# Kernel optimization log

Hardware: AMD Instinct MI355X
Metric: run time of the kernel (lower is better)

## Reference

```python
import jax, jax.numpy as jnp
import numpy as np

B, C, H, W = 8, 512, 32, 32


def setup_inputs() -> dict:
    key = jax.random.key(0)
    ks = jax.random.split(key, 7)
    s = 0.02  # typical conv init scale
    return {
        "x": jax.random.normal(ks[0], (B, C, H, W), dtype=jnp.float32),
        "Wq": jax.random.normal(ks[1], (C, C), dtype=jnp.float32) * s,
        "bq": jax.random.normal(ks[2], (C,), dtype=jnp.float32) * s,
        "Wk": jax.random.normal(ks[3], (C, C), dtype=jnp.float32) * s,
        "bk": jax.random.normal(ks[4], (C,), dtype=jnp.float32) * s,
        "W6": jax.random.normal(ks[5], (C, C), dtype=jnp.float32) * s,
        "b6": jax.random.normal(ks[6], (C,), dtype=jnp.float32) * s,
    }


def _gam(x, Wq, bq, Wk, bk, W6, b6):
    b, c, h, w = x.shape
    hw = h * w
    scale = 1.0 / (c ** 0.5)
    # 1x1 convs == per-pixel channel matmuls (torch conv weight [out,in,1,1])
    q = jnp.einsum('bchw,dc->bhwd', x, Wq) + bq          # [B,H,W,C]
    q = q.reshape(b * hw, c)                              # query rows
    k = jnp.einsum('bchw,dc->bdhw', x, Wk) + bk[None, :, None, None]
    k = jnp.transpose(k, (1, 0, 2, 3)).reshape(c, b * hw)  # [C, B*HW]
    xw = (q.astype(jnp.float32) @ k.astype(jnp.float32))   # [B*HW, B*HW]
    xw = xw.reshape(b * hw, b, hw)
    xw = jnp.max(xw, axis=-1)                              # max over keys' spatial dim
    xw = jnp.mean(xw, axis=-1)                             # mean over key images
    xw = xw.reshape(b, hw) * scale
    xw = jax.nn.softmax(xw, axis=-1).astype(x.dtype)
    xw = xw.reshape(b, 1, h, w)
    x5 = x * xw
    return jnp.einsum('bchw,dc->bdhw', x5, W6) + b6[None, :, None, None]


def reference(x, Wq, bq, Wk, bk, W6, b6):
    x_new = _gam(x, Wq, bq, Wk, bk, W6, b6)
    # prototype: mean over batch and spatial dims, keep channels
    x_proto = jnp.mean(x_new.astype(jnp.float32), axis=(0, 2, 3)).astype(x.dtype)
    return x * x_proto[None, :, None, None]
```

## Files before the change

### kernel.cpp

```cpp
#include <hip/hip_runtime.h>
#include <hip/hip_bf16.h>

typedef __bf16 bf16_t;
typedef __bf16 bf16x8 __attribute__((ext_vector_type(8)));
typedef float f32x4 __attribute__((ext_vector_type(4)));

#define B_   8
#define C_   512
#define HW_  1024
#define NPIX 8192

typedef __attribute__((address_space(3))) void lds_vp;
typedef const __attribute__((address_space(1))) void gbl_vp;
__device__ __forceinline__ void gload_lds16(const void* g, void* l) {
    __builtin_amdgcn_global_load_lds((gbl_vp*)g, (lds_vp*)l, 16, 0, 0);
}

__device__ __forceinline__ void stage128x64_swz(const bf16_t* __restrict__ g,
                                                bf16_t* lds, int tid) {
    int w64 = tid & ~63;
#pragma unroll
    for (int s = 0; s < 4; ++s) {
        int u = s * 256 + tid;
        int row = u >> 3;
        int kg = (u & 7) ^ (row & 7);
        const bf16_t* src = g + (size_t)row * 512 + kg * 8;
        gload_lds16((const void*)src, (void*)(lds + (size_t)(s * 256 + w64) * 8));
    }
}

__global__ void k_transpose(const float* __restrict__ x, bf16_t* __restrict__ xT,
                            const float* __restrict__ Wq, const float* __restrict__ Wk,
                            bf16_t* __restrict__ wq, bf16_t* __restrict__ wk) {
    __shared__ bf16_t tile[64 * 66];
    int p0 = blockIdx.x * 64, c0 = blockIdx.y * 64, b = blockIdx.z;
    int t = threadIdx.x;
    int widx = ((blockIdx.z * 8 + blockIdx.y) * 16 + blockIdx.x) * 256 + t;
    wq[widx] = (bf16_t)Wq[widx];
    wk[widx] = (bf16_t)Wk[widx];
#pragma unroll
    for (int s = 0; s < 16; ++s) {
        int u = s * 256 + t;
        int cr = u >> 6, pc = u & 63;
        tile[cr * 66 + pc] = (bf16_t)x[((size_t)(b * C_ + c0 + cr)) * HW_ + p0 + pc];
    }
    __syncthreads();
#pragma unroll
    for (int s = 0; s < 16; ++s) {
        int u = s * 256 + t;
        int pr = u >> 6, cc = u & 63;
        xT[((size_t)(b * HW_ + p0 + pr)) * C_ + c0 + cc] = tile[cc * 66 + pr];
    }
}

__launch_bounds__(256, 2)
__global__ void k_gemm_qk(const bf16_t* __restrict__ xT,
                          const bf16_t* __restrict__ wq, const bf16_t* __restrict__ wk,
                          const float* __restrict__ bq, const float* __restrict__ bk,
                          bf16_t* __restrict__ qo, bf16_t* __restrict__ ko) {
    __shared__ __align__(16) bf16_t As[128 * 64];
    __shared__ __align__(16) bf16_t Bs[128 * 64];
    int bid = blockIdx.x;
    int mtile = bid >> 3;
    int nt = bid & 7;
    const bf16_t* wsel = (nt < 4) ? wq : wk;
    const float*  bsel = (nt < 4) ? bq : bk;
    bf16_t*       osel = (nt < 4) ? qo : ko;
    int nb = (nt & 3) * 128;
    int i0 = mtile * 128;
    int tid = threadIdx.x;
    int lane = tid & 63, w = tid >> 6;
    int wr = w >> 1, wc = w & 1, lr = lane & 15, lg = lane >> 4;
    int kswz = (lg ^ (lr & 7)) << 4;

    f32x4 acc[4][4];
#pragma unroll
    for (int mi = 0; mi < 4; ++mi)
#pragma unroll
        for (int ni = 0; ni < 4; ++ni)
#pragma unroll
            for (int r = 0; r < 4; ++r) acc[mi][ni][r] = 0.f;

    for (int kt = 0; kt < 8; ++kt) {
        int k0 = kt * 64;
        stage128x64_swz(xT + (size_t)i0 * 512 + k0, As, tid);
        stage128x64_swz(wsel + (size_t)nb * 512 + k0, Bs, tid);
        asm volatile("s_waitcnt vmcnt(0)" ::: "memory");
        __builtin_amdgcn_s_barrier();
#pragma unroll
        for (int kk = 0; kk < 2; ++kk) {
            bf16x8 af[4], bfr[4];
#pragma unroll
            for (int mi = 0; mi < 4; ++mi)
                af[mi] = *(const bf16x8*)((const char*)As +
                    (wr * 64 + mi * 16 + lr) * 128 + (kswz ^ (kk * 64)));
#pragma unroll
            for (int ni = 0; ni < 4; ++ni)
                bfr[ni] = *(const bf16x8*)((const char*)Bs +
                    (wc * 64 + ni * 16 + lr) * 128 + (kswz ^ (kk * 64)));
#pragma unroll
            for (int mi = 0; mi < 4; ++mi)
#pragma unroll
                for (int ni = 0; ni < 4; ++ni)
                    acc[mi][ni] = __builtin_amdgcn_mfma_f32_16x16x32_bf16(
                        af[mi], bfr[ni], acc[mi][ni], 0, 0, 0);
        }
        __builtin_amdgcn_s_barrier();
    }
#pragma unroll
    for (int ni = 0; ni < 4; ++ni) {
        int col = nb + wc * 64 + ni * 16 + lr;
        float bias = bsel[col];
#pragma unroll
        for (int mi = 0; mi < 4; ++mi) {
            int rowb = i0 + wr * 64 + mi * 16 + lg * 4;
#pragma unroll
            for (int r = 0; r < 4; ++r)
                osel[(size_t)(rowb + r) * 512 + col] = (bf16_t)(acc[mi][ni][r] + bias);
        }
    }
}


#define STAGE_A(RH, D, T)                                                          \
    gload_lds16((const void*)(q + srcA + (size_t)((RH) * 128) * 512 +              \
                              ((T) & 7) * 64),                                     \
                (void*)(ldsb + (RH) * 32768 + (D) * 16384 + ldw));                 \
    gload_lds16((const void*)(q + srcA + (size_t)((RH) * 128 + 64) * 512 +         \
                              ((T) & 7) * 64),                                     \
                (void*)(ldsb + (RH) * 32768 + (D) * 16384 + 8192 + ldw));

#define STAGE_B(RH, D, T)                                                          \
    gload_lds16((const void*)(kb + srcB +                                          \
                              (size_t)(((T) >> 3) * 256 + (RH) * 128) * 512 +      \
                              ((T) & 7) * 64),                                     \
                (void*)(ldsb + 65536 + (RH) * 32768 + (D) * 16384 + ldw));         \
    gload_lds16((const void*)(kb + srcB +                                          \
                              (size_t)(((T) >> 3) * 256 + (RH) * 128 + 64) * 512 + \
                              ((T) & 7) * 64),                                     \
                (void*)(ldsb + 65536 + (RH) * 32768 + (D) * 16384 + 8192 + ldw));

#define PHASE(D, KH, MH, STAGE_STMT, VM_STMT)                                      \
    {                                                                              \
        const char* Ab = ldsb + wr * 32768 + (D) * 16384;                          \
        const char* Bb = ldsb + 65536 + (wc >> 1) * 32768 + (D) * 16384;           \
        _Pragma("unroll")                                                          \
        for (int mi = 0; mi < 4; ++mi)                                             \
            af[mi] = *(const bf16x8*)(Ab + (aswz ^ ((KH) * 64)) +                  \
                                      ((MH) * 4 + mi) * 2048);                     \
        if ((MH) == 0) {                                                           \
            _Pragma("unroll")                                                      \
            for (int ni = 0; ni < 4; ++ni)                                         \
                bf[ni] = *(const bf16x8*)(Bb + (bswz ^ ((KH) * 64)) + ni * 2048);  \
        }                                                                          \
        STAGE_STMT;                                                                \
        __builtin_amdgcn_s_setprio(1);                                             \
        _Pragma("unroll")                                                          \
        for (int mi = 0; mi < 4; ++mi)                                             \
            _Pragma("unroll")                                                      \
            for (int ni = 0; ni < 4; ++ni)                                         \
                acc[(MH) * 4 + mi][ni] = __builtin_amdgcn_mfma_f32_16x16x32_bf16(  \
                    af[mi], bf[ni], acc[(MH) * 4 + mi][ni], 0, 0, 0);              \
        __builtin_amdgcn_s_setprio(0);                                             \
        VM_STMT;                                                                   \
        __builtin_amdgcn_s_barrier();                                              \
    }

__global__ __launch_bounds__(512, 2)
void k_gemm_max8(const bf16_t* __restrict__ q, const bf16_t* __restrict__ kp,
                 float* __restrict__ Mout) {
    __shared__ __align__(16) bf16_t lds[65536];
    char* ldsb = (char*)lds;
    int bid = blockIdx.x;
    int img = bid & 7;
    int qp = bid >> 3;
    int i0 = qp * 256;
    const bf16_t* kb = kp + (size_t)img * HW_ * C_;
    int tid = threadIdx.x;
    int lane = tid & 63, w = tid >> 6;
    int wr = w >> 2, wc = w & 3;
    int lr = lane & 15, lg = lane >> 4;
    int kswz = (lg ^ (lr & 7)) << 4;
    int aswz = lr * 128 + kswz;
    int bswz = ((wc & 1) * 64 + lr) * 128 + kswz;

    int srow = tid >> 3;
    int sk = (((tid & 7) ^ ((tid >> 3) & 7))) << 3;
    size_t srcA = (size_t)(i0 + srow) * 512 + sk;
    size_t srcB = (size_t)srow * 512 + sk;
    int ldw = (tid >> 6) * 1024;

    f32x4 acc[8][4];
    bf16x8 af[4], bf[4];
    float rm[8][4];
#pragma unroll
    for (int mi = 0; mi < 8; ++mi)
#pragma unroll
        for (int ni = 0; ni < 4; ++ni)
#pragma unroll
            for (int r = 0; r < 4; ++r) acc[mi][ni][r] = 0.f;
#pragma unroll
    for (int mi = 0; mi < 8; ++mi)
#pragma unroll
        for (int r = 0; r < 4; ++r) rm[mi][r] = -3.4e38f;

    STAGE_B(0, 0, 0) STAGE_A(0, 0, 0) STAGE_B(1, 0, 0) STAGE_A(1, 0, 0)
    STAGE_B(0, 1, 1)
    asm volatile("s_waitcnt vmcnt(2)" ::: "memory");
    __builtin_amdgcn_s_barrier();

    for (int i = 0; i < 16; ++i) {
        int tb = 2 * i + 1, tc = 2 * i + 2, td = 2 * i + 3;
        bool s = (i < 15);
        PHASE(0, 0, 0, { STAGE_A(0, 1, tb) }, {})
        PHASE(0, 0, 1, { STAGE_B(1, 1, tb) }, {})
        PHASE(0, 1, 0, { STAGE_A(1, 1, tb) }, {})
        PHASE(0, 1, 1, { if (s) { STAGE_B(0, 0, tc) } },
              { if (s) { asm volatile("s_waitcnt vmcnt(2)" ::: "memory"); }
                else   { asm volatile("s_waitcnt vmcnt(0)" ::: "memory"); } })
        PHASE(1, 0, 0, { if (s) { STAGE_A(0, 0, tc) } }, {})
        PHASE(1, 0, 1, { if (s) { STAGE_B(1, 0, tc) } }, {})
        PHASE(1, 1, 0, { if (s) { STAGE_A(1, 0, tc) } }, {})
        PHASE(1, 1, 1, { if (s) { STAGE_B(0, 1, td) } },
              { if (s) { asm volatile("s_waitcnt vmcnt(2)" ::: "memory"); } })
        if ((i & 3) == 3) {
#pragma unroll
            for (int mi = 0; mi < 8; ++mi)
#pragma unroll
                for (int r = 0; r < 4; ++r) {
                    float v = fmaxf(fmaxf(acc[mi][0][r], acc[mi][1][r]),
                                    fmaxf(acc[mi][2][r], acc[mi][3][r]));
                    rm[mi][r] = fmaxf(rm[mi][r], v);
#pragma unroll
                    for (int ni = 0; ni < 4; ++ni) acc[mi][ni][r] = 0.f;
                }
        }
    }

#pragma unroll
    for (int mi = 0; mi < 8; ++mi)
#pragma unroll
        for (int r = 0; r < 4; ++r) {
            float v = rm[mi][r];
#pragma unroll
            for (int off = 1; off < 16; off <<= 1) v = fmaxf(v, __shfl_xor(v, off));
            rm[mi][r] = v;
        }
    float* sm = (float*)lds;
    if (lr == 0) {
#pragma unroll
        for (int mi = 0; mi < 8; ++mi)
#pragma unroll
            for (int r = 0; r < 4; ++r)
                sm[wc * 256 + wr * 128 + mi * 16 + lg * 4 + r] = rm[mi][r];
    }
    __syncthreads();
    if (tid < 256) {
        float v = fmaxf(fmaxf(sm[tid], sm[256 + tid]),
                        fmaxf(sm[512 + tid], sm[768 + tid]));
        Mout[(size_t)(i0 + tid) * 8 + img] = v;
    }
}

__global__ void k_softmax(const float* __restrict__ Mout, float* __restrict__ wsm) {
    int b = blockIdx.x;
    int t = threadIdx.x;
    __shared__ float red[16];
    const float scale = 0.044194173824159216f;
    float s[4];
#pragma unroll
    for (int i = 0; i < 4; ++i) {
        int p = t + i * 256;
        const float* row = &Mout[(size_t)(b * 1024 + p) * 8];
        float acc = 0.f;
#pragma unroll
        for (int j = 0; j < 8; ++j) acc += row[j];
        s[i] = acc * (scale / 8.0f);
    }
    float m = fmaxf(fmaxf(s[0], s[1]), fmaxf(s[2], s[3]));
#pragma unroll
    for (int off = 1; off < 64; off <<= 1) m = fmaxf(m, __shfl_xor(m, off));
    if ((t & 63) == 0) red[t >> 6] = m;
    __syncthreads();
    float m4 = fmaxf(fmaxf(red[0], red[1]), fmaxf(red[2], red[3]));
    float e[4], sum = 0.f;
#pragma unroll
    for (int i = 0; i < 4; ++i) { e[i] = __expf(s[i] - m4); sum += e[i]; }
#pragma unroll
    for (int off = 1; off < 64; off <<= 1) sum += __shfl_xor(sum, off);
    if ((t & 63) == 0) red[8 + (t >> 6)] = sum;
    __syncthreads();
    float tot = red[8] + red[9] + red[10] + red[11];
    float inv = 1.0f / tot;
#pragma unroll
    for (int i = 0; i < 4; ++i) wsm[b * 1024 + t + i * 256] = e[i] * inv;
}

__global__ void k_reduce_y(const float* __restrict__ x, const float* __restrict__ wsm,
                           float* __restrict__ y) {
    int c = blockIdx.x;
    int t = threadIdx.x;
    float acc = 0.f;
    for (int b = 0; b < 8; ++b) {
        const float* xb = x + ((size_t)(b * C_ + c)) * HW_;
        const float* wb = wsm + b * HW_;
#pragma unroll
        for (int i = 0; i < 4; ++i) {
            int p = t + i * 256;
            acc += xb[p] * wb[p];
        }
    }
#pragma unroll
    for (int off = 1; off < 64; off <<= 1) acc += __shfl_xor(acc, off);
    __shared__ float red[4];
    if ((t & 63) == 0) red[t >> 6] = acc;
    __syncthreads();
    if (t == 0) y[c] = (red[0] + red[1] + red[2] + red[3]) * (1.0f / 8192.0f);
}

__global__ void k_proto(const float* __restrict__ W6, const float* __restrict__ b6,
                        const float* __restrict__ y, float* __restrict__ proto) {
    int d = blockIdx.x;
    int lane = threadIdx.x;
    float acc = 0.f;
#pragma unroll
    for (int i = 0; i < 8; ++i)
        acc += W6[(size_t)d * C_ + lane + i * 64] * y[lane + i * 64];
#pragma unroll
    for (int off = 1; off < 64; off <<= 1) acc += __shfl_xor(acc, off);
    if (lane == 0) proto[d] = acc + b6[d];
}

__global__ void k_final(const float* __restrict__ x, const float* __restrict__ proto,
                        float* __restrict__ out) {
    int idx = blockIdx.x * 256 + threadIdx.x;
    float4 v = ((const float4*)x)[idx];
    int c = (idx >> 8) & 511;
    float p = proto[c];
    v.x *= p; v.y *= p; v.z *= p; v.w *= p;
    ((float4*)out)[idx] = v;
}

extern "C" void kernel_launch(void* const* d_in, const int* in_sizes, int n_in,
                              void* d_out, int out_size, void* d_ws, size_t ws_size,
                              hipStream_t stream) {
    const float* x  = (const float*)d_in[0];
    const float* Wq = (const float*)d_in[1];
    const float* bq = (const float*)d_in[2];
    const float* Wk = (const float*)d_in[3];
    const float* bk = (const float*)d_in[4];
    const float* W6 = (const float*)d_in[5];
    const float* b6 = (const float*)d_in[6];
    float* out = (float*)d_out;

    char* ws = (char*)d_ws;
    bf16_t* xT    = (bf16_t*)(ws);
    float*  Mout  = (float*)(ws);
    bf16_t* wqb   = (bf16_t*)(ws + 8388608);
    bf16_t* wkb   = (bf16_t*)(ws + 8912896);
    bf16_t* qb    = (bf16_t*)(ws + 9437184);
    bf16_t* kb    = (bf16_t*)(ws + 17825792);
    float*  wsm   = (float*)(ws + 26476544);
    float*  yv    = (float*)(ws + 26509312);
    float*  proto = (float*)(ws + 26511360);

    hipLaunchKernelGGL(k_transpose, dim3(16, 8, 8), dim3(256), 0, stream,
                       x, xT, Wq, Wk, wqb, wkb);
    hipLaunchKernelGGL(k_gemm_qk, dim3(512), dim3(256), 0, stream,
                       xT, wqb, wkb, bq, bk, qb, kb);
    hipLaunchKernelGGL(k_gemm_max8, dim3(256), dim3(512), 0, stream, qb, kb, Mout);
    hipLaunchKernelGGL(k_softmax, dim3(8), dim3(256), 0, stream, Mout, wsm);
    hipLaunchKernelGGL(k_reduce_y, dim3(512), dim3(256), 0, stream, x, wsm, yv);
    hipLaunchKernelGGL(k_proto, dim3(512), dim3(64), 0, stream, W6, b6, yv, proto);
    hipLaunchKernelGGL(k_final, dim3(4096), dim3(256), 0, stream, x, proto, out);
}
```

Baseline: 96.13 us.

## Reuse pipelined 256x256 GEMM macros for Q/K projection and vectorize transpose

Replaces the simple 128x128 single-buffered Q/K projection GEMM with a 256x256-tile, 512-thread kernel. It reuses the double-buffered STAGE/PHASE macros from the max GEMM, so global-to-LDS loads overlap with MFMA work. The transpose kernel now uses float4 loads and bf16x4 stores with a 65-stride LDS tile. The larger tiles launch only 128 blocks, which may underfill the GPU's compute units.

```diff
diff --git a/kernel.cpp b/kernel.cpp
--- a/kernel.cpp
+++ b/kernel.cpp
@@ -3,6 +3,7 @@
 
 typedef __bf16 bf16_t;
 typedef __bf16 bf16x8 __attribute__((ext_vector_type(8)));
+typedef __bf16 bf16x4 __attribute__((ext_vector_type(4)));
 typedef float f32x4 __attribute__((ext_vector_type(4)));
 
 #define B_   8
@@ -16,108 +17,36 @@
     __builtin_amdgcn_global_load_lds((gbl_vp*)g, (lds_vp*)l, 16, 0, 0);
 }
 
-__device__ __forceinline__ void stage128x64_swz(const bf16_t* __restrict__ g,
-                                                bf16_t* lds, int tid) {
-    int w64 = tid & ~63;
-#pragma unroll
-    for (int s = 0; s < 4; ++s) {
-        int u = s * 256 + tid;
-        int row = u >> 3;
-        int kg = (u & 7) ^ (row & 7);
-        const bf16_t* src = g + (size_t)row * 512 + kg * 8;
-        gload_lds16((const void*)src, (void*)(lds + (size_t)(s * 256 + w64) * 8));
-    }
-}
-
 __global__ void k_transpose(const float* __restrict__ x, bf16_t* __restrict__ xT,
                             const float* __restrict__ Wq, const float* __restrict__ Wk,
                             bf16_t* __restrict__ wq, bf16_t* __restrict__ wk) {
-    __shared__ bf16_t tile[64 * 66];
+    __shared__ bf16_t tile[64 * 65];
     int p0 = blockIdx.x * 64, c0 = blockIdx.y * 64, b = blockIdx.z;
     int t = threadIdx.x;
     int widx = ((blockIdx.z * 8 + blockIdx.y) * 16 + blockIdx.x) * 256 + t;
     wq[widx] = (bf16_t)Wq[widx];
     wk[widx] = (bf16_t)Wk[widx];
 #pragma unroll
-    for (int s = 0; s < 16; ++s) {
+    for (int s = 0; s < 4; ++s) {
         int u = s * 256 + t;
-        int cr = u >> 6, pc = u & 63;
-        tile[cr * 66 + pc] = (bf16_t)x[((size_t)(b * C_ + c0 + cr)) * HW_ + p0 + pc];
-    }
-    __syncthreads();
-#pragma unroll
-    for (int s = 0; s < 16; ++s) {
+        int cr = u >> 4, pc = (u & 15) * 4;
+        float4 v = *(const float4*)&x[((size_t)(b * C_ + c0 + cr)) * HW_ + p0 + pc];
+        tile[cr * 65 + pc + 0] = (bf16_t)v.x;
+        tile[cr * 65 + pc + 1] = (bf16_t)v.y;
+        tile[cr * 65 + pc + 2] = (bf16_t)v.z;
+        tile[cr * 65 + pc + 3] = (bf16_t)v.w;
+    }
+    __syncthreads();
+#pragma unroll
+    for (int s = 0; s < 4; ++s) {
         int u = s * 256 + t;
-        int pr = u >> 6, cc = u & 63;
-        xT[((size_t)(b * HW_ + p0 + pr)) * C_ + c0 + cc] = tile[cc * 66 + pr];
-    }
-}
-
-__launch_bounds__(256, 2)
-__global__ void k_gemm_qk(const bf16_t* __restrict__ xT,
-                          const bf16_t* __restrict__ wq, const bf16_t* __restrict__ wk,
-                          const float* __restrict__ bq, const float* __restrict__ bk,
-                          bf16_t* __restrict__ qo, bf16_t* __restrict__ ko) {
-    __shared__ __align__(16) bf16_t As[128 * 64];
-    __shared__ __align__(16) bf16_t Bs[128 * 64];
-    int bid = blockIdx.x;
-    int mtile = bid >> 3;
-    int nt = bid & 7;
-    const bf16_t* wsel = (nt < 4) ? wq : wk;
-    const float*  bsel = (nt < 4) ? bq : bk;
-    bf16_t*       osel = (nt < 4) ? qo : ko;
-    int nb = (nt & 3) * 128;
-    int i0 = mtile * 128;
-    int tid = threadIdx.x;
-    int lane = tid & 63, w = tid >> 6;
-    int wr = w >> 1, wc = w & 1, lr = lane & 15, lg = lane >> 4;
-    int kswz = (lg ^ (lr & 7)) << 4;
-
-    f32x4 acc[4][4];
-#pragma unroll
-    for (int mi = 0; mi < 4; ++mi)
-#pragma unroll
-        for (int ni = 0; ni < 4; ++ni)
-#pragma unroll
-            for (int r = 0; r < 4; ++r) acc[mi][ni][r] = 0.f;
-
-    for (int kt = 0; kt < 8; ++kt) {
-        int k0 = kt * 64;
-        stage128x64_swz(xT + (size_t)i0 * 512 + k0, As, tid);
-        stage128x64_swz(wsel + (size_t)nb * 512 + k0, Bs, tid);
-        asm volatile("s_waitcnt vmcnt(0)" ::: "memory");
-        __builtin_amdgcn_s_barrier();
-#pragma unroll
-        for (int kk = 0; kk < 2; ++kk) {
-            bf16x8 af[4], bfr[4];
-#pragma unroll
-            for (int mi = 0; mi < 4; ++mi)
-                af[mi] = *(const bf16x8*)((const char*)As +
-                    (wr * 64 + mi * 16 + lr) * 128 + (kswz ^ (kk * 64)));
-#pragma unroll
-            for (int ni = 0; ni < 4; ++ni)
-                bfr[ni] = *(const bf16x8*)((const char*)Bs +
-                    (wc * 64 + ni * 16 + lr) * 128 + (kswz ^ (kk * 64)));
-#pragma unroll
-            for (int mi = 0; mi < 4; ++mi)
-#pragma unroll
-                for (int ni = 0; ni < 4; ++ni)
-                    acc[mi][ni] = __builtin_amdgcn_mfma_f32_16x16x32_bf16(
-                        af[mi], bfr[ni], acc[mi][ni], 0, 0, 0);
-        }
-        __builtin_amdgcn_s_barrier();
-    }
-#pragma unroll
-    for (int ni = 0; ni < 4; ++ni) {
-        int col = nb + wc * 64 + ni * 16 + lr;
-        float bias = bsel[col];
-#pragma unroll
-        for (int mi = 0; mi < 4; ++mi) {
-            int rowb = i0 + wr * 64 + mi * 16 + lg * 4;
-#pragma unroll
-            for (int r = 0; r < 4; ++r)
-                osel[(size_t)(rowb + r) * 512 + col] = (bf16_t)(acc[mi][ni][r] + bias);
-        }
+        int pr = u >> 4, cc = (u & 15) * 4;
+        bf16x4 o;
+        o[0] = tile[(cc + 0) * 65 + pr];
+        o[1] = tile[(cc + 1) * 65 + pr];
+        o[2] = tile[(cc + 2) * 65 + pr];
+        o[3] = tile[(cc + 3) * 65 + pr];
+        *(bf16x4*)&xT[((size_t)(b * HW_ + p0 + pr)) * C_ + c0 + cc] = o;
     }
 }
 
@@ -167,6 +96,81 @@
     }
 
 __global__ __launch_bounds__(512, 2)
+void k_gemm_qk8(const bf16_t* __restrict__ xT,
+                const bf16_t* __restrict__ wqb, const bf16_t* __restrict__ wkb,
+                const float* __restrict__ bq, const float* __restrict__ bk,
+                bf16_t* __restrict__ qo, bf16_t* __restrict__ ko) {
+    __shared__ __align__(16) bf16_t lds[65536];
+    char* ldsb = (char*)lds;
+    int bid = blockIdx.x;
+    int ntile = bid & 3;
+    int mtile = bid >> 2;
+    int i0 = mtile * 256;
+    const bf16_t* q = xT;
+    const bf16_t* kb = ((ntile < 2) ? wqb : wkb) + (size_t)(ntile & 1) * 256 * 512;
+    const float* bsel = ((ntile < 2) ? bq : bk) + (ntile & 1) * 256;
+    bf16_t* osel = (ntile < 2) ? qo : ko;
+    int cb = (ntile & 1) * 256;
+    int tid = threadIdx.x;
+    int lane = tid & 63, w = tid >> 6;
+    int wr = w >> 2, wc = w & 3;
+    int lr = lane & 15, lg = lane >> 4;
+    int kswz = (lg ^ (lr & 7)) << 4;
+    int aswz = lr * 128 + kswz;
+    int bswz = ((wc & 1) * 64 + lr) * 128 + kswz;
+
+    int srow = tid >> 3;
+    int sk = (((tid & 7) ^ ((tid >> 3) & 7))) << 3;
+    size_t srcA = (size_t)(i0 + srow) * 512 + sk;
+    size_t srcB = (size_t)srow * 512 + sk;
+    int ldw = (tid >> 6) * 1024;
+
+    f32x4 acc[8][4];
+    bf16x8 af[4], bf[4];
+#pragma unroll
+    for (int mi = 0; mi < 8; ++mi)
+#pragma unroll
+        for (int ni = 0; ni < 4; ++ni)
+#pragma unroll
+            for (int r = 0; r < 4; ++r) acc[mi][ni][r] = 0.f;
+
+    STAGE_B(0, 0, 0) STAGE_A(0, 0, 0) STAGE_B(1, 0, 0) STAGE_A(1, 0, 0)
+    STAGE_B(0, 1, 1)
+    asm volatile("s_waitcnt vmcnt(2)" ::: "memory");
+    __builtin_amdgcn_s_barrier();
+
+    for (int i = 0; i < 4; ++i) {
+        int tb = 2 * i + 1, tc = 2 * i + 2, td = 2 * i + 3;
+        bool s = (i < 3);
+        PHASE(0, 0, 0, { STAGE_A(0, 1, tb) }, {})
+        PHASE(0, 0, 1, { STAGE_B(1, 1, tb) }, {})
+        PHASE(0, 1, 0, { STAGE_A(1, 1, tb) }, {})
+        PHASE(0, 1, 1, { if (s) { STAGE_B(0, 0, tc) } },
+              { if (s) { asm volatile("s_waitcnt vmcnt(2)" ::: "memory"); }
+                else   { asm volatile("s_waitcnt vmcnt(0)" ::: "memory"); } })
+        PHASE(1, 0, 0, { if (s) { STAGE_A(0, 0, tc) } }, {})
+        PHASE(1, 0, 1, { if (s) { STAGE_B(1, 0, tc) } }, {})
+        PHASE(1, 1, 0, { if (s) { STAGE_A(1, 0, tc) } }, {})
+        PHASE(1, 1, 1, { if (s) { STAGE_B(0, 1, td) } },
+              { if (s) { asm volatile("s_waitcnt vmcnt(2)" ::: "memory"); } })
+    }
+
+#pragma unroll
+    for (int ni = 0; ni < 4; ++ni) {
+        int colL = wc * 64 + ni * 16 + lr;
+        float bias = bsel[colL];
+#pragma unroll
+        for (int mi = 0; mi < 8; ++mi) {
+            int rowb = i0 + wr * 128 + mi * 16 + lg * 4;
+#pragma unroll
+            for (int r = 0; r < 4; ++r)
+                osel[(size_t)(rowb + r) * 512 + cb + colL] =
+                    (bf16_t)(acc[mi][ni][r] + bias);
+        }
+    }
+}
+
+__global__ __launch_bounds__(512, 2)
 void k_gemm_max8(const bf16_t* __restrict__ q, const bf16_t* __restrict__ kp,
                  float* __restrict__ Mout) {
     __shared__ __align__(16) bf16_t lds[65536];
@@ -366,7 +370,7 @@
 
     hipLaunchKernelGGL(k_transpose, dim3(16, 8, 8), dim3(256), 0, stream,
                        x, xT, Wq, Wk, wqb, wkb);
-    hipLaunchKernelGGL(k_gemm_qk, dim3(512), dim3(256), 0, stream,
+    hipLaunchKernelGGL(k_gemm_qk8, dim3(128), dim3(512), 0, stream,
                        xT, wqb, wkb, bq, bk, qb, kb);
     hipLaunchKernelGGL(k_gemm_max8, dim3(256), dim3(512), 0, stream, qb, kb, Mout);
     hipLaunchKernelGGL(k_softmax, dim3(8), dim3(256), 0, stream, Mout, wsm);
```

New measurement: 99.52 us. +3.5%, slower.
